# Performance work log

Measured on AMD Instinct MI355X. Metric: run time of the kernel, lower is better.

## Reference

```python
import jax, jax.numpy as jnp
import numpy as np

N_NODES = 10000
HEADS = 4
NEG_SLOPE = 0.2


def gat_conv(x, src, dst, W, att_src, att_dst, bias, heads, ch):
    # x: [N, F_in]; W: [F_in, heads*ch]; att_*: [heads, ch]; bias: [heads*ch]
    N = x.shape[0]
    h = (x @ W).reshape(N, heads, ch)                       # [N, H, C]
    a_s = jnp.einsum('nhc,hc->nh', h, att_src)              # [N, H]
    a_d = jnp.einsum('nhc,hc->nh', h, att_dst)              # [N, H]
    e = jax.nn.leaky_relu(a_s[src] + a_d[dst], NEG_SLOPE)   # [E, H]
    # segment softmax over incoming edges of each dst node
    m = jax.ops.segment_max(e, dst, num_segments=N)         # [N, H]
    e = jnp.exp(e - m[dst])
    denom = jax.ops.segment_sum(e, dst, num_segments=N)     # [N, H]
    alpha = e / (denom[dst] + 1e-16)                        # [E, H]
    msg = h[src] * alpha[:, :, None]                        # [E, H, C]
    out = jax.ops.segment_sum(msg, dst, num_segments=N)     # [N, H, C]
    return out.reshape(N, heads * ch) + bias                # concat heads


def setup_inputs() -> dict:
    key = jax.random.key(0)
    ks = jax.random.split(key, 12)
    in_c, hid, out_c, H = 256, 64, 64, HEADS
    n_edges = 320000
    x = jax.random.normal(ks[0], (N_NODES, in_c), dtype=jnp.float32)
    edge_index = jax.random.randint(ks[1], (2, n_edges), 0, N_NODES, dtype=jnp.int64)

    def glorot(k, shape):
        fan = shape[0] + shape[-1]
        s = jnp.sqrt(6.0 / fan)
        return jax.random.uniform(k, shape, jnp.float32, -s, s)

    return {
        'x': x, 'edge_index': edge_index,
        'W1': glorot(ks[2], (in_c, H * hid)),
        'a1s': glorot(ks[3], (H, hid)), 'a1d': glorot(ks[4], (H, hid)),
        'b1': jnp.zeros((H * hid,), jnp.float32),
        'W2': glorot(ks[5], (H * hid, H * hid)),
        'a2s': glorot(ks[6], (H, hid)), 'a2d': glorot(ks[7], (H, hid)),
        'b2': jnp.zeros((H * hid,), jnp.float32),
        'W3': glorot(ks[8], (H * hid, H * out_c)),
        'a3s': glorot(ks[9], (H, out_c)), 'a3d': glorot(ks[10], (H, out_c)),
        'b3': jnp.zeros((H * out_c,), jnp.float32),
    }


def reference(x, edge_index, W1, a1s, a1d, b1, W2, a2s, a2d, b2, W3, a3s, a3d, b3):
    N = x.shape[0]
    # PyG GATConv default: add self loops
    loops = jnp.arange(N, dtype=edge_index.dtype)
    src = jnp.concatenate([edge_index[0], loops])
    dst = jnp.concatenate([edge_index[1], loops])
    hid, out_c = 64, 64
    h1 = jax.nn.elu(gat_conv(x, src, dst, W1, a1s, a1d, b1, HEADS, hid))
    h2 = jax.nn.elu(gat_conv(h1, src, dst, W2, a2s, a2d, b2, HEADS, hid))
    oup = jax.nn.elu(gat_conv(h2, src, dst, W3, a3s, a3d, b3, HEADS, out_c))
    return oup
```

## Files before the change

### kernel.cpp

```cpp
#include <hip/hip_runtime.h>
#include <hip/hip_bf16.h>

typedef __hip_bfloat16 bf16;
typedef __bf16 bf16x8v __attribute__((ext_vector_type(8)));
typedef float f32x4 __attribute__((ext_vector_type(4)));
typedef unsigned short u16x8 __attribute__((ext_vector_type(8)));

#define CAP 128

__device__ __forceinline__ float bits2f(unsigned short u) {
  union { unsigned int i; float f; } c;
  c.i = ((unsigned int)u) << 16;
  return c.f;
}


template <bool FP32IN, bool WF32>
__device__ __forceinline__ void gemm_body(const void* __restrict__ Xv,
                                          const void* __restrict__ Wv,
                                          const float* __restrict__ att_s,
                                          const float* __restrict__ att_d,
                                          bf16* __restrict__ H, float* __restrict__ a_s,
                                          float* __restrict__ a_d, int M, int m0, int hd,
                                          bf16* As, bf16* Bs) {
  const int LDK = 136;
  int tid = threadIdx.x;
  int wave = tid >> 6, lane = tid & 63;
  int quad = lane >> 4, l16 = lane & 15;
  int n0 = hd * 64;
  int srow = tid >> 2;
  int koff = (tid & 3) * 32;

  const float* Xf = (const float*)Xv;
  const bf16*  Xb = (const bf16*)Xv;
  const float* Wf = (const float*)Wv;
  const bf16*  Wb = (const bf16*)Wv;

  f32x4 acc[4] = {{0.f, 0.f, 0.f, 0.f}, {0.f, 0.f, 0.f, 0.f},
                  {0.f, 0.f, 0.f, 0.f}, {0.f, 0.f, 0.f, 0.f}};

  for (int ks = 0; ks < 256; ks += 128) {
    int gm = m0 + srow;
#pragma unroll
    for (int c = 0; c < 4; c++) {
      int ko = koff + c * 8;
      uint4 v;
      if (FP32IN) {
        float4 u0 = make_float4(0.f, 0.f, 0.f, 0.f), u1 = u0;
        if (gm < M) {
          u0 = *(const float4*)&Xf[gm * 256 + ks + ko];
          u1 = *(const float4*)&Xf[gm * 256 + ks + ko + 4];
        }
        union { bf16 h[8]; uint4 u; } pk;
        pk.h[0] = __float2bfloat16(u0.x); pk.h[1] = __float2bfloat16(u0.y);
        pk.h[2] = __float2bfloat16(u0.z); pk.h[3] = __float2bfloat16(u0.w);
        pk.h[4] = __float2bfloat16(u1.x); pk.h[5] = __float2bfloat16(u1.y);
        pk.h[6] = __float2bfloat16(u1.z); pk.h[7] = __float2bfloat16(u1.w);
        v = pk.u;
      } else {
        v = (gm < M) ? *(const uint4*)&Xb[gm * 256 + ks + ko]
                     : make_uint4(0u, 0u, 0u, 0u);
      }
      *(uint4*)&As[srow * LDK + ko] = v;
    }
    if (WF32) {
      int tn = tid & 63, kq = tid >> 6;
#pragma unroll
      for (int i = 0; i < 32; i++) {
        int kk2 = kq * 32 + i;
        Bs[tn * LDK + kk2] = __float2bfloat16(Wf[(size_t)(ks + kk2) * 256 + n0 + tn]);
      }
    } else {
#pragma unroll
      for (int c = 0; c < 4; c++) {
        int ko = koff + c * 8;
        *(uint4*)&Bs[srow * LDK + ko] = *(const uint4*)&Wb[(n0 + srow) * 256 + ks + ko];
      }
    }
    __syncthreads();

#pragma unroll
    for (int kk = 0; kk < 4; kk++) {
      bf16x8v af = *(const bf16x8v*)&As[(wave * 16 + l16) * LDK + kk * 32 + quad * 8];
#pragma unroll
      for (int t = 0; t < 4; t++) {
        bf16x8v bfr = *(const bf16x8v*)&Bs[(t * 16 + l16) * LDK + kk * 32 + quad * 8];
        acc[t] = __builtin_amdgcn_mfma_f32_16x16x32_bf16(af, bfr, acc[t], 0, 0, 0);
      }
    }
    __syncthreads();
  }

  float ps[4] = {0.f, 0.f, 0.f, 0.f}, pd[4] = {0.f, 0.f, 0.f, 0.f};
#pragma unroll
  for (int t = 0; t < 4; t++) {
    float sa = att_s[hd * 64 + t * 16 + l16];
    float da = att_d[hd * 64 + t * 16 + l16];
#pragma unroll
    for (int j = 0; j < 4; j++) {
      int gm = m0 + wave * 16 + quad * 4 + j;
      float v = acc[t][j];
      if (gm < M) H[gm * 256 + n0 + t * 16 + l16] = __float2bfloat16(v);
      ps[j] += v * sa;
      pd[j] += v * da;
    }
  }
#pragma unroll
  for (int j = 0; j < 4; j++) {
#pragma unroll
    for (int s = 1; s < 16; s <<= 1) {
      ps[j] += __shfl_xor(ps[j], s, 64);
      pd[j] += __shfl_xor(pd[j], s, 64);
    }
    int gm = m0 + wave * 16 + quad * 4 + j;
    if (l16 == 0 && gm < M) {
      a_s[gm * 4 + hd] = ps[j];
      a_d[gm * 4 + hd] = pd[j];
    }
  }
}

__global__ void __launch_bounds__(256, 4)
gemm_mfma_kernel(const bf16* __restrict__ X, const bf16* __restrict__ Wt,
                 const float* __restrict__ att_s, const float* __restrict__ att_d,
                 bf16* __restrict__ H, float* __restrict__ a_s, float* __restrict__ a_d,
                 int M) {
  __shared__ bf16 As[64 * 136];
  __shared__ bf16 Bs[64 * 136];
  gemm_body<false, false>(X, Wt, att_s, att_d, H, a_s, a_d, M, blockIdx.x * 64,
                          blockIdx.y, As, Bs);
}

__global__ void __launch_bounds__(256, 4)
gemm1_fill_kernel(const float* __restrict__ X, const float* __restrict__ W0,
                  const float* __restrict__ att_s, const float* __restrict__ att_d,
                  bf16* __restrict__ H, float* __restrict__ a_s, float* __restrict__ a_d,
                  int M, const int* __restrict__ ei, int E, int N,
                  int* __restrict__ cnt, int* __restrict__ csr, int ngb, int eb,
                  const float* __restrict__ W1, const float* __restrict__ W2,
                  bf16* __restrict__ Wt) {
  __shared__ bf16 As[64 * 136];
  __shared__ bf16 Bs[64 * 136];
  __shared__ float tile[16][17];
  int b = blockIdx.x;
  if (b < ngb) {
    gemm_body<true, true>(X, W0, att_s, att_d, H, a_s, a_d, M, (b >> 2) * 64, b & 3,
                          As, Bs);
  } else if (b < ngb + eb) {
    int t = (b - ngb) * 256 + threadIdx.x;
    if (t >= E + N) return;
    int src, dst;
    if (t < E) { src = ei[t]; dst = ei[E + t]; }
    else       { src = t - E; dst = t - E; }
    int pos = atomicAdd(&cnt[dst], 1);
    if (pos < CAP) csr[dst * CAP + pos] = src;
  } else {
    int b2 = b - ngb - eb;
    int L = 1 + (b2 >> 8), rem = b2 & 255;
    const float* W = (L == 1) ? W1 : W2;
    bf16* T = Wt + (size_t)L * 65536;
    int n0 = (rem & 15) * 16, k0 = (rem >> 4) * 16;
    int tx = threadIdx.x & 15, ty = threadIdx.x >> 4;
    tile[ty][tx] = W[(k0 + ty) * 256 + n0 + tx];
    __syncthreads();
    T[(n0 + ty) * 256 + k0 + tx] = __float2bfloat16(tile[tx][ty]);
  }
}


template <bool FINAL>
__global__ void __launch_bounds__(256, 8)
agg_wave_kernel(const bf16* __restrict__ H, const float* __restrict__ a_s,
                const float* __restrict__ a_d, const int* __restrict__ cnt,
                const int* __restrict__ csr, const float* __restrict__ bias,
                bf16* __restrict__ OutB, float* __restrict__ OutF, int N) {
  __shared__ int   wIdxS[4][128];
  __shared__ float wPS[4][512];
  int tid = threadIdx.x;
  int wave = tid >> 6, lane = tid & 63;
  int n = blockIdx.x * 4 + wave;
  int* wIdx = wIdxS[wave];
  float* wP = wPS[wave];
  if (n >= N) return;

  int deg = min(cnt[n], CAP);
  int degp = (deg + 7) & ~7;
  {
    float4 ad4 = *(const float4*)&a_d[n * 4];
#pragma unroll
    for (int base = 0; base < 2; base++) {
      int jj = base * 64 + lane;
      if (jj < deg) {
        int src = csr[n * CAP + jj];
        wIdx[jj] = src;
        float4 as4 = *(const float4*)&a_s[src * 4];
        float4 e;
        e.x = as4.x + ad4.x; e.x = (e.x > 0.f) ? e.x : 0.2f * e.x;
        e.y = as4.y + ad4.y; e.y = (e.y > 0.f) ? e.y : 0.2f * e.y;
        e.z = as4.z + ad4.z; e.z = (e.z > 0.f) ? e.z : 0.2f * e.z;
        e.w = as4.w + ad4.w; e.w = (e.w > 0.f) ? e.w : 0.2f * e.w;
        float4 pv;
        pv.x = __expf(e.x); pv.y = __expf(e.y);
        pv.z = __expf(e.z); pv.w = __expf(e.w);
        *(float4*)&wP[jj * 4] = pv;
      }
    }
    int pad = degp - deg;
    if (lane < pad) {
      wIdx[deg + lane] = 0;
      *(float4*)&wP[(deg + lane) * 4] = make_float4(0.f, 0.f, 0.f, 0.f);
    }
  }
  asm volatile("s_waitcnt lgkmcnt(0)" ::: "memory");
  __builtin_amdgcn_sched_barrier(0);

  int sel = lane >> 5;
  int l32 = lane & 31;
  int c8 = l32 * 8;
  int head = l32 >> 3;
  const unsigned short* Hs = (const unsigned short*)H;

  float acc[8] = {0.f, 0.f, 0.f, 0.f, 0.f, 0.f, 0.f, 0.f};
  float s = 0.f;
  int npairp = degp >> 1;

  for (int it = 0; it < npairp; it += 4) {
    int jv[4]; int sv[4]; float pv[4]; u16x8 hv[4];
#pragma unroll
    for (int u = 0; u < 4; u++) jv[u] = 2 * (it + u) + sel;
#pragma unroll
    for (int u = 0; u < 4; u++) sv[u] = wIdx[jv[u]];
#pragma unroll
    for (int u = 0; u < 4; u++) pv[u] = wP[jv[u] * 4 + head];
#pragma unroll
    for (int u = 0; u < 4; u++) hv[u] = *(const u16x8*)(Hs + sv[u] * 256 + c8);
#pragma unroll
    for (int u = 0; u < 4; u++) {
      s += pv[u];
#pragma unroll
      for (int k = 0; k < 8; k++) acc[k] += pv[u] * bits2f(hv[u][k]);
    }
  }

  s += __shfl_xor(s, 32, 64);
#pragma unroll
  for (int k = 0; k < 8; k++) acc[k] += __shfl_xor(acc[k], 32, 64);

  if (sel == 0) {
    float inv = 1.f / (s + 1e-16f);
    float4 b0 = *(const float4*)&bias[c8];
    float4 b1 = *(const float4*)&bias[c8 + 4];
    float v[8];
    v[0] = acc[0] * inv + b0.x; v[1] = acc[1] * inv + b0.y;
    v[2] = acc[2] * inv + b0.z; v[3] = acc[3] * inv + b0.w;
    v[4] = acc[4] * inv + b1.x; v[5] = acc[5] * inv + b1.y;
    v[6] = acc[6] * inv + b1.z; v[7] = acc[7] * inv + b1.w;
#pragma unroll
    for (int k = 0; k < 8; k++) v[k] = (v[k] > 0.f) ? v[k] : expm1f(v[k]);
    if (FINAL) {
      *(float4*)&OutF[n * 256 + c8]     = make_float4(v[0], v[1], v[2], v[3]);
      *(float4*)&OutF[n * 256 + c8 + 4] = make_float4(v[4], v[5], v[6], v[7]);
    } else {
      union { bf16 h[8]; u16x8 u; } pk;
#pragma unroll
      for (int k = 0; k < 8; k++) pk.h[k] = __float2bfloat16(v[k]);
      *(u16x8*)((unsigned short*)OutB + n * 256 + c8) = pk.u;
    }
  }
}


extern "C" void kernel_launch(void* const* d_in, const int* in_sizes, int n_in,
                              void* d_out, int out_size, void* d_ws, size_t ws_size,
                              hipStream_t stream) {
  const int N = in_sizes[0] / 256;
  const int E = in_sizes[1] / 2;

  const float* x  = (const float*)d_in[0];
  const int*   ei = (const int*)d_in[1];
  const float* Wl[3]  = {(const float*)d_in[2], (const float*)d_in[6], (const float*)d_in[10]};
  const float* asl[3] = {(const float*)d_in[3], (const float*)d_in[7], (const float*)d_in[11]};
  const float* adl[3] = {(const float*)d_in[4], (const float*)d_in[8], (const float*)d_in[12]};
  const float* bl[3]  = {(const float*)d_in[5], (const float*)d_in[9], (const float*)d_in[13]};
  float* out = (float*)d_out;

  char* p = (char*)d_ws;
  auto carve = [&](size_t bytes) {
    char* r = p;
    p += (bytes + 255) & ~size_t(255);
    return r;
  };
  int*   cnt   = (int*)carve(sizeof(int) * N);
  int*   csr   = (int*)carve(sizeof(int) * N * CAP);
  float* a_s   = (float*)carve(sizeof(float) * N * 4);
  float* a_d   = (float*)carve(sizeof(float) * N * 4);
  bf16*  Wt    = (bf16*)carve(sizeof(bf16) * 3 * 65536);
  bf16*  h_buf = (bf16*)carve(sizeof(bf16) * N * 256);
  bf16*  x_buf = (bf16*)carve(sizeof(bf16) * N * 256);
  (void)ws_size; (void)n_in; (void)out_size;

  const int eb  = (E + N + 255) / 256;
  const int ngb = ((N + 63) / 64) * 4;
  const int ab  = (N + 3) / 4;
  dim3 ggrid((N + 63) / 64, 4);

  hipMemsetAsync(cnt, 0, sizeof(int) * N, stream);
  gemm1_fill_kernel<<<ngb + eb + 512, 256, 0, stream>>>(
      x, Wl[0], asl[0], adl[0], h_buf, a_s, a_d, N, ei, E, N, cnt, csr, ngb, eb,
      Wl[1], Wl[2], Wt);
  agg_wave_kernel<false><<<ab, 256, 0, stream>>>(h_buf, a_s, a_d, cnt, csr, bl[0],
                                                 x_buf, nullptr, N);
  gemm_mfma_kernel<<<ggrid, 256, 0, stream>>>(x_buf, Wt + 65536, asl[1], adl[1],
                                              h_buf, a_s, a_d, N);
  agg_wave_kernel<false><<<ab, 256, 0, stream>>>(h_buf, a_s, a_d, cnt, csr, bl[1],
                                                 x_buf, nullptr, N);
  gemm_mfma_kernel<<<ggrid, 256, 0, stream>>>(x_buf, Wt + 131072, asl[2], adl[2],
                                              h_buf, a_s, a_d, N);
  agg_wave_kernel<true><<<ab, 256, 0, stream>>>(h_buf, a_s, a_d, cnt, csr, bl[2],
                                                nullptr, out, N);
}
```

Before: 189.8 us.

## Split aggregation into four edge groups over two half-row passes

Restructures the per-node aggregation loop. Four 16-lane groups now each handle a different edge, and every 256-byte half of the bf16 feature row is covered in one of two passes. Before, two 32-lane halves each covered a full 512-byte row. The aim is more independent gathers in flight per wave and finer tail handling (steps of 4 edges instead of 16). The cost is reading wIdx/wP twice, extra shuffle reductions, and the output store being split into two passes. It also switches the bf16 output store to a nontemporal store.

```diff
diff --git a/kernel.cpp b/kernel.cpp
--- a/kernel.cpp
+++ b/kernel.cpp
@@ -214,57 +214,76 @@
   asm volatile("s_waitcnt lgkmcnt(0)" ::: "memory");
   __builtin_amdgcn_sched_barrier(0);
 
-  int sel = lane >> 5;
-  int l32 = lane & 31;
-  int c8 = l32 * 8;
-  int head = l32 >> 3;
-  const unsigned short* Hs = (const unsigned short*)H;
-
-  float acc[8] = {0.f, 0.f, 0.f, 0.f, 0.f, 0.f, 0.f, 0.f};
-  float s = 0.f;
-  int npairp = degp >> 1;
-
-  for (int it = 0; it < npairp; it += 4) {
-    int jv[4]; int sv[4]; float pv[4]; u16x8 hv[4];
-#pragma unroll
-    for (int u = 0; u < 4; u++) jv[u] = 2 * (it + u) + sel;
-#pragma unroll
-    for (int u = 0; u < 4; u++) sv[u] = wIdx[jv[u]];
-#pragma unroll
-    for (int u = 0; u < 4; u++) pv[u] = wP[jv[u] * 4 + head];
-#pragma unroll
-    for (int u = 0; u < 4; u++) hv[u] = *(const u16x8*)(Hs + sv[u] * 256 + c8);
-#pragma unroll
-    for (int u = 0; u < 4; u++) {
-      s += pv[u];
-#pragma unroll
-      for (int k = 0; k < 8; k++) acc[k] += pv[u] * bits2f(hv[u][k]);
-    }
-  }
-
-  s += __shfl_xor(s, 32, 64);
-#pragma unroll
-  for (int k = 0; k < 8; k++) acc[k] += __shfl_xor(acc[k], 32, 64);
-
-  if (sel == 0) {
-    float inv = 1.f / (s + 1e-16f);
-    float4 b0 = *(const float4*)&bias[c8];
-    float4 b1 = *(const float4*)&bias[c8 + 4];
-    float v[8];
-    v[0] = acc[0] * inv + b0.x; v[1] = acc[1] * inv + b0.y;
-    v[2] = acc[2] * inv + b0.z; v[3] = acc[3] * inv + b0.w;
-    v[4] = acc[4] * inv + b1.x; v[5] = acc[5] * inv + b1.y;
-    v[6] = acc[6] * inv + b1.z; v[7] = acc[7] * inv + b1.w;
-#pragma unroll
-    for (int k = 0; k < 8; k++) v[k] = (v[k] > 0.f) ? v[k] : expm1f(v[k]);
-    if (FINAL) {
-      *(float4*)&OutF[n * 256 + c8]     = make_float4(v[0], v[1], v[2], v[3]);
-      *(float4*)&OutF[n * 256 + c8 + 4] = make_float4(v[4], v[5], v[6], v[7]);
-    } else {
-      union { bf16 h[8]; u16x8 u; } pk;
-#pragma unroll
-      for (int k = 0; k < 8; k++) pk.h[k] = __float2bfloat16(v[k]);
-      *(u16x8*)((unsigned short*)OutB + n * 256 + c8) = pk.u;
+  int grp = lane >> 4;
+  int l16 = lane & 15;
+  const char* Hb = (const char*)H;
+
+#pragma unroll 2
+  for (int p = 0; p < 2; p++) {
+    int hd = p * 2 + (l16 >> 3);
+    int boff = p * 256 + l16 * 16;
+    float acc[8] = {0.f, 0.f, 0.f, 0.f, 0.f, 0.f, 0.f, 0.f};
+    float s = 0.f;
+
+    int j = 0;
+    for (; j + 16 <= degp; j += 16) {
+      int sv[4]; float pv[4]; u16x8 hv[4];
+#pragma unroll
+      for (int u = 0; u < 4; u++) {
+        int e = j + u * 4 + grp;
+        sv[u] = wIdx[e];
+        pv[u] = wP[e * 4 + hd];
+      }
+#pragma unroll
+      for (int u = 0; u < 4; u++)
+        hv[u] = *(const u16x8*)(Hb + ((size_t)sv[u] << 9) + boff);
+#pragma unroll
+      for (int u = 0; u < 4; u++) {
+        s += pv[u];
+#pragma unroll
+        for (int k = 0; k < 8; k++) acc[k] += pv[u] * bits2f(hv[u][k]);
+      }
+    }
+    for (; j < degp; j += 4) {
+      int e = j + grp;
+      int sv0 = wIdx[e];
+      float pv0 = wP[e * 4 + hd];
+      u16x8 hv0 = *(const u16x8*)(Hb + ((size_t)sv0 << 9) + boff);
+      s += pv0;
+#pragma unroll
+      for (int k = 0; k < 8; k++) acc[k] += pv0 * bits2f(hv0[k]);
+    }
+
+    s += __shfl_xor(s, 16, 64);
+    s += __shfl_xor(s, 32, 64);
+#pragma unroll
+    for (int k = 0; k < 8; k++) {
+      acc[k] += __shfl_xor(acc[k], 16, 64);
+      acc[k] += __shfl_xor(acc[k], 32, 64);
+    }
+
+    if (grp == 0) {
+      int c0 = p * 128 + l16 * 8;
+      float inv = 1.f / (s + 1e-16f);
+      float4 b0 = *(const float4*)&bias[c0];
+      float4 b1 = *(const float4*)&bias[c0 + 4];
+      float v[8];
+      v[0] = acc[0] * inv + b0.x; v[1] = acc[1] * inv + b0.y;
+      v[2] = acc[2] * inv + b0.z; v[3] = acc[3] * inv + b0.w;
+      v[4] = acc[4] * inv + b1.x; v[5] = acc[5] * inv + b1.y;
+      v[6] = acc[6] * inv + b1.z; v[7] = acc[7] * inv + b1.w;
+#pragma unroll
+      for (int k = 0; k < 8; k++) v[k] = (v[k] > 0.f) ? v[k] : expm1f(v[k]);
+      if (FINAL) {
+        *(float4*)&OutF[n * 256 + c0]     = make_float4(v[0], v[1], v[2], v[3]);
+        *(float4*)&OutF[n * 256 + c0 + 4] = make_float4(v[4], v[5], v[6], v[7]);
+      } else {
+        union { bf16 h[8]; u16x8 u; } pk;
+#pragma unroll
+        for (int k = 0; k < 8; k++) pk.h[k] = __float2bfloat16(v[k]);
+        __builtin_nontemporal_store(
+            pk.u, (u16x8*)((unsigned short*)OutB + n * 256 + c0));
+      }
     }
   }
 }
```

Result: slower. 199.6 us (+5.2%).
